# Kernel optimization log

Measured on AMD Instinct MI355X. Metric: run time of the kernel, lower is better.

## Reference

```python
import jax, jax.numpy as jnp
import numpy as np

OUT, IN = 4096, 4096  # W_shape
K, BLOCK = 256, 8     # codebook entries, block dim


def setup_inputs() -> dict:
    key = jax.random.key(0)
    k1, k2, k3, k4, k5 = jax.random.split(key, 5)
    x = jax.random.normal(k1, (4, 2048, IN), dtype=jnp.float32)
    centroids = jax.random.normal(k2, (K, BLOCK), dtype=jnp.float32)
    labels = jax.random.randint(k3, (OUT * IN // BLOCK,), 0, K, dtype=jnp.int64)
    scale = jax.random.uniform(k4, (IN,), dtype=jnp.float32)
    bias = jax.random.normal(k5, (OUT,), dtype=jnp.float32)
    return {"x": x, "centroids": centroids, "labels": labels, "scale": scale, "bias": bias}


def reference(x, centroids, labels, scale, bias):
    # VQ weight decompression: gather codebook vectors, reshape to [OUT, IN]
    W_smooth = centroids[labels].reshape(OUT, IN)
    # F.linear(x * scale, W, bias) == (x*scale) @ W.T + bias
    return jnp.einsum('bsi,oi->bso', x * scale, W_smooth) + bias
```

## Files before the change

### kernel.cpp

```cpp
#include <hip/hip_runtime.h>
#include <stdint.h>

#define M_DIM 8192
#define N_DIM 4096
#define K_DIM 4096
#define NUM_VQ (N_DIM * K_DIM / 8)
#define NUM_X  (M_DIM * K_DIM)

typedef __attribute__((ext_vector_type(4))) float f32x4;
typedef __attribute__((ext_vector_type(8))) short bf16x8;
typedef unsigned short u16;

__device__ inline unsigned short f2bf(float f) {
    union { float f; unsigned int i; } v; v.f = f;
    unsigned int x = v.i;
    return (unsigned short)((x + 0x7FFFu + ((x >> 16) & 1u)) >> 16);
}

__global__ void detect_i64(const int* __restrict__ labels, int* __restrict__ flag) {
    if (threadIdx.x == 0) {
        int is64 = 1;
        for (int i = 1; i < 128; i += 2)
            if (labels[i] != 0) { is64 = 0; break; }
        *flag = is64;
    }
}

__global__ void convert_x(const float* __restrict__ x, u16* __restrict__ xb) {
    int i = blockIdx.x * blockDim.x + threadIdx.x;
    f32x4 a = ((const f32x4*)x)[2 * i];
    f32x4 b = ((const f32x4*)x)[2 * i + 1];
    bf16x8 o;
#pragma unroll
    for (int j = 0; j < 4; ++j) { o[j] = (short)f2bf(a[j]); o[4 + j] = (short)f2bf(b[j]); }
    ((bf16x8*)xb)[i] = o;
}

__global__ void decompress(const int* __restrict__ labels,
                           const float* __restrict__ centroids,
                           const float* __restrict__ scale,
                           u16* __restrict__ Ws,
                           const int* __restrict__ flag) {
    int i = blockIdx.x * blockDim.x + threadIdx.x;
    int lab = (*flag) ? labels[2 * i] : labels[i];
    int kb = i & 511;
    f32x4 c0 = ((const f32x4*)centroids)[2 * lab];
    f32x4 c1 = ((const f32x4*)centroids)[2 * lab + 1];
    f32x4 s0 = ((const f32x4*)scale)[2 * kb];
    f32x4 s1 = ((const f32x4*)scale)[2 * kb + 1];
    bf16x8 o;
#pragma unroll
    for (int j = 0; j < 4; ++j) {
        o[j]     = (short)f2bf(c0[j] * s0[j]);
        o[4 + j] = (short)f2bf(c1[j] * s1[j]);
    }
    ((bf16x8*)Ws)[i] = o;
}

__global__ __launch_bounds__(256)
void gemm_bias(const u16* __restrict__ A, const u16* __restrict__ B,
               const float* __restrict__ bias, float* __restrict__ C) {
    __shared__ u16 ldsA[128 * 32];
    __shared__ u16 ldsB[128 * 32];

    const int tid  = threadIdx.x;
    const int wave = tid >> 6;
    const int lane = tid & 63;
    const int bm = blockIdx.y * 128;
    const int bn = blockIdx.x * 128;

    const int srow = wave * 32 + (lane >> 2);
    const int scol = (lane & 3) * 8;
    const u16* gA = A + (size_t)(bm + srow) * K_DIM + scol;
    const u16* gB = B + (size_t)(bn + srow) * K_DIM + scol;
    u16* lA = ldsA + wave * 1024;
    u16* lB = ldsB + wave * 1024;

    const int wm = (wave >> 1) * 64;
    const int wn = (wave & 1) * 64;
    const int fm = lane & 15;
    const int fk = (lane >> 4) * 8;

    f32x4 acc[4][4];
#pragma unroll
    for (int i = 0; i < 4; ++i)
#pragma unroll
        for (int j = 0; j < 4; ++j)
            acc[i][j] = (f32x4){0.f, 0.f, 0.f, 0.f};

    for (int kt = 0; kt < K_DIM / 32; ++kt) {
        __builtin_amdgcn_global_load_lds(
            (const __attribute__((address_space(1))) void*)gA,
            (__attribute__((address_space(3))) void*)lA, 16, 0, 0);
        __builtin_amdgcn_global_load_lds(
            (const __attribute__((address_space(1))) void*)(gA + 16 * K_DIM),
            (__attribute__((address_space(3))) void*)(lA + 512), 16, 0, 0);
        __builtin_amdgcn_global_load_lds(
            (const __attribute__((address_space(1))) void*)gB,
            (__attribute__((address_space(3))) void*)lB, 16, 0, 0);
        __builtin_amdgcn_global_load_lds(
            (const __attribute__((address_space(1))) void*)(gB + 16 * K_DIM),
            (__attribute__((address_space(3))) void*)(lB + 512), 16, 0, 0);
        gA += 32;
        gB += 32;
        __syncthreads();

        bf16x8 af[4], bfr[4];
#pragma unroll
        for (int i = 0; i < 4; ++i)
            af[i] = *(const bf16x8*)&ldsA[(wm + i * 16 + fm) * 32 + fk];
#pragma unroll
        for (int j = 0; j < 4; ++j)
            bfr[j] = *(const bf16x8*)&ldsB[(wn + j * 16 + fm) * 32 + fk];

#pragma unroll
        for (int i = 0; i < 4; ++i)
#pragma unroll
            for (int j = 0; j < 4; ++j)
                acc[i][j] = __builtin_amdgcn_mfma_f32_16x16x32_bf16(
                    af[i], bfr[j], acc[i][j], 0, 0, 0);
        __syncthreads();
    }

    float biasv[4];
#pragma unroll
    for (int j = 0; j < 4; ++j)
        biasv[j] = bias[bn + wn + j * 16 + (lane & 15)];

    const int crow0 = bm + wm + (lane >> 4) * 4;
    const int ccol0 = bn + wn + (lane & 15);
#pragma unroll
    for (int i = 0; i < 4; ++i)
#pragma unroll
        for (int r = 0; r < 4; ++r) {
            size_t rowoff = (size_t)(crow0 + i * 16 + r) * N_DIM;
#pragma unroll
            for (int j = 0; j < 4; ++j)
                C[rowoff + ccol0 + j * 16] = acc[i][j][r] + biasv[j];
        }
}

__global__ __launch_bounds__(256)
void gemm_bias_cvtA(const float* __restrict__ A32, const u16* __restrict__ B,
                    const float* __restrict__ bias, float* __restrict__ C) {
    __shared__ u16 ldsA[128 * 32];
    __shared__ u16 ldsB[128 * 32];

    const int tid  = threadIdx.x;
    const int wave = tid >> 6;
    const int lane = tid & 63;
    const int bm = blockIdx.y * 128;
    const int bn = blockIdx.x * 128;

    const int srow = wave * 32 + (lane >> 2);
    const int scol = (lane & 3) * 8;
    const float* gA = A32 + (size_t)(bm + srow) * K_DIM + scol;
    const u16*   gB = B   + (size_t)(bn + srow) * K_DIM + scol;
    u16* lA = ldsA + wave * 1024;
    u16* lB = ldsB + wave * 1024;
    const int ldst = lane * 8;

    const int wm = (wave >> 1) * 64;
    const int wn = (wave & 1) * 64;
    const int fm = lane & 15;
    const int fk = (lane >> 4) * 8;

    f32x4 acc[4][4];
#pragma unroll
    for (int i = 0; i < 4; ++i)
#pragma unroll
        for (int j = 0; j < 4; ++j)
            acc[i][j] = (f32x4){0.f, 0.f, 0.f, 0.f};

    for (int kt = 0; kt < K_DIM / 32; ++kt) {
        f32x4 a0 = *(const f32x4*)gA;
        f32x4 a1 = *(const f32x4*)(gA + 4);
        f32x4 a2 = *(const f32x4*)(gA + 16 * K_DIM);
        f32x4 a3 = *(const f32x4*)(gA + 16 * K_DIM + 4);
        __builtin_amdgcn_global_load_lds(
            (const __attribute__((address_space(1))) void*)gB,
            (__attribute__((address_space(3))) void*)lB, 16, 0, 0);
        __builtin_amdgcn_global_load_lds(
            (const __attribute__((address_space(1))) void*)(gB + 16 * K_DIM),
            (__attribute__((address_space(3))) void*)(lB + 512), 16, 0, 0);
        bf16x8 p0, p1;
#pragma unroll
        for (int j = 0; j < 4; ++j) {
            p0[j] = (short)f2bf(a0[j]); p0[4 + j] = (short)f2bf(a1[j]);
            p1[j] = (short)f2bf(a2[j]); p1[4 + j] = (short)f2bf(a3[j]);
        }
        *(bf16x8*)&lA[ldst]       = p0;
        *(bf16x8*)&lA[ldst + 512] = p1;
        gA += 32;
        gB += 32;
        __syncthreads();

        bf16x8 af[4], bfr[4];
#pragma unroll
        for (int i = 0; i < 4; ++i)
            af[i] = *(const bf16x8*)&ldsA[(wm + i * 16 + fm) * 32 + fk];
#pragma unroll
        for (int j = 0; j < 4; ++j)
            bfr[j] = *(const bf16x8*)&ldsB[(wn + j * 16 + fm) * 32 + fk];

#pragma unroll
        for (int i = 0; i < 4; ++i)
#pragma unroll
            for (int j = 0; j < 4; ++j)
                acc[i][j] = __builtin_amdgcn_mfma_f32_16x16x32_bf16(
                    af[i], bfr[j], acc[i][j], 0, 0, 0);
        __syncthreads();
    }

    float biasv[4];
#pragma unroll
    for (int j = 0; j < 4; ++j)
        biasv[j] = bias[bn + wn + j * 16 + (lane & 15)];

    const int crow0 = bm + wm + (lane >> 4) * 4;
    const int ccol0 = bn + wn + (lane & 15);
#pragma unroll
    for (int i = 0; i < 4; ++i)
#pragma unroll
        for (int r = 0; r < 4; ++r) {
            size_t rowoff = (size_t)(crow0 + i * 16 + r) * N_DIM;
#pragma unroll
            for (int j = 0; j < 4; ++j)
                C[rowoff + ccol0 + j * 16] = acc[i][j][r] + biasv[j];
        }
}

extern "C" void kernel_launch(void* const* d_in, const int* in_sizes, int n_in,
                              void* d_out, int out_size, void* d_ws, size_t ws_size,
                              hipStream_t stream) {
    const float* x         = (const float*)d_in[0];
    const float* centroids = (const float*)d_in[1];
    const int*   labels    = (const int*)d_in[2];
    const float* scale     = (const float*)d_in[3];
    const float* bias      = (const float*)d_in[4];
    float* out             = (float*)d_out;

    int* flag = (int*)d_ws;
    u16* Ws   = (u16*)((char*)d_ws + 256);
    u16* Xb   = (u16*)((char*)d_ws + 256 + (size_t)NUM_VQ * 16);

    const size_t need_full = 256 + (size_t)NUM_VQ * 16 + (size_t)NUM_X * 2;
    const size_t need_ws   = 256 + (size_t)NUM_VQ * 16;

    detect_i64<<<1, 64, 0, stream>>>(labels, flag);
    decompress<<<NUM_VQ / 256, 256, 0, stream>>>(labels, centroids, scale, Ws, flag);

    dim3 grid(N_DIM / 128, M_DIM / 128);
    if (ws_size >= need_full) {
        convert_x<<<NUM_X / 8 / 256, 256, 0, stream>>>(x, Xb);
        gemm_bias<<<grid, 256, 0, stream>>>(Xb, Ws, bias, out);
    } else if (ws_size >= need_ws) {
        gemm_bias_cvtA<<<grid, 256, 0, stream>>>(x, Ws, bias, out);
    }
}
```

Before: 536.6 us.

## Swizzle GEMM LDS layout, merge prep kernels, parallelize label-width detect

Applies an XOR swizzle to the column chunk each lane writes into LDS via global_load_lds, and a matching swizzle on the fragment reads, to cut LDS bank conflicts in the MFMA inner loop. It also merges weight decompression and x-to-bf16 conversion into one prep launch, and uses a wave ballot for int64 label detection. The workspace-size fallback path (cvtA GEMM) is removed, so the kernel now assumes a workspace large enough for the bf16 copy of x.

```diff
diff --git a/kernel.cpp b/kernel.cpp
--- a/kernel.cpp
+++ b/kernel.cpp
@@ -6,6 +6,8 @@
 #define K_DIM 4096
 #define NUM_VQ (N_DIM * K_DIM / 8)
 #define NUM_X  (M_DIM * K_DIM)
+#define VQ_BLOCKS (NUM_VQ / 256)
+#define CVT_BLOCKS (NUM_X / 8 / 256)
 
 typedef __attribute__((ext_vector_type(4))) float f32x4;
 typedef __attribute__((ext_vector_type(8))) short bf16x8;
@@ -18,43 +20,42 @@
 }
 
 __global__ void detect_i64(const int* __restrict__ labels, int* __restrict__ flag) {
-    if (threadIdx.x == 0) {
-        int is64 = 1;
-        for (int i = 1; i < 128; i += 2)
-            if (labels[i] != 0) { is64 = 0; break; }
-        *flag = is64;
-    }
+    int v = labels[2 * threadIdx.x + 1];
+    unsigned long long nz = __ballot(v != 0);
+    if (threadIdx.x == 0) *flag = (nz == 0ull) ? 1 : 0;
 }
 
-__global__ void convert_x(const float* __restrict__ x, u16* __restrict__ xb) {
-    int i = blockIdx.x * blockDim.x + threadIdx.x;
-    f32x4 a = ((const f32x4*)x)[2 * i];
-    f32x4 b = ((const f32x4*)x)[2 * i + 1];
-    bf16x8 o;
+__global__ void prep(const int* __restrict__ labels,
+                     const float* __restrict__ centroids,
+                     const float* __restrict__ scale,
+                     const float* __restrict__ x,
+                     u16* __restrict__ Ws, u16* __restrict__ Xb,
+                     const int* __restrict__ flag) {
+    int b = blockIdx.x;
+    if (b < VQ_BLOCKS) {
+        int i = b * 256 + threadIdx.x;
+        int lab = (*flag) ? labels[2 * i] : labels[i];
+        int kb = i & 511;
+        f32x4 c0 = ((const f32x4*)centroids)[2 * lab];
+        f32x4 c1 = ((const f32x4*)centroids)[2 * lab + 1];
+        f32x4 s0 = ((const f32x4*)scale)[2 * kb];
+        f32x4 s1 = ((const f32x4*)scale)[2 * kb + 1];
+        bf16x8 o;
 #pragma unroll
-    for (int j = 0; j < 4; ++j) { o[j] = (short)f2bf(a[j]); o[4 + j] = (short)f2bf(b[j]); }
-    ((bf16x8*)xb)[i] = o;
-}
-
-__global__ void decompress(const int* __restrict__ labels,
-                           const float* __restrict__ centroids,
-                           const float* __restrict__ scale,
-                           u16* __restrict__ Ws,
-                           const int* __restrict__ flag) {
-    int i = blockIdx.x * blockDim.x + threadIdx.x;
-    int lab = (*flag) ? labels[2 * i] : labels[i];
-    int kb = i & 511;
-    f32x4 c0 = ((const f32x4*)centroids)[2 * lab];
-    f32x4 c1 = ((const f32x4*)centroids)[2 * lab + 1];
-    f32x4 s0 = ((const f32x4*)scale)[2 * kb];
-    f32x4 s1 = ((const f32x4*)scale)[2 * kb + 1];
-    bf16x8 o;
+        for (int j = 0; j < 4; ++j) {
+            o[j]     = (short)f2bf(c0[j] * s0[j]);
+            o[4 + j] = (short)f2bf(c1[j] * s1[j]);
+        }
+        ((bf16x8*)Ws)[i] = o;
+    } else {
+        int i = (b - VQ_BLOCKS) * 256 + threadIdx.x;
+        f32x4 a = ((const f32x4*)x)[2 * i];
+        f32x4 c = ((const f32x4*)x)[2 * i + 1];
+        bf16x8 o;
 #pragma unroll
-    for (int j = 0; j < 4; ++j) {
-        o[j]     = (short)f2bf(c0[j] * s0[j]);
-        o[4 + j] = (short)f2bf(c1[j] * s1[j]);
+        for (int j = 0; j < 4; ++j) { o[j] = (short)f2bf(a[j]); o[4 + j] = (short)f2bf(c[j]); }
+        ((bf16x8*)Xb)[i] = o;
     }
-    ((bf16x8*)Ws)[i] = o;
 }
 
 __global__ __launch_bounds__(256)
@@ -70,7 +71,7 @@
     const int bn = blockIdx.x * 128;
 
     const int srow = wave * 32 + (lane >> 2);
-    const int scol = (lane & 3) * 8;
+    const int scol = (((lane & 3) ^ ((lane >> 3) & 3))) * 8;
     const u16* gA = A + (size_t)(bm + srow) * K_DIM + scol;
     const u16* gB = B + (size_t)(bn + srow) * K_DIM + scol;
     u16* lA = ldsA + wave * 1024;
@@ -79,7 +80,7 @@
     const int wm = (wave >> 1) * 64;
     const int wn = (wave & 1) * 64;
     const int fm = lane & 15;
-    const int fk = (lane >> 4) * 8;
+    const int fks = (((lane >> 4) ^ ((lane >> 1) & 3)) & 3) * 8;
 
     f32x4 acc[4][4];
 #pragma unroll
@@ -108,100 +109,10 @@
         bf16x8 af[4], bfr[4];
 #pragma unroll
         for (int i = 0; i < 4; ++i)
-            af[i] = *(const bf16x8*)&ldsA[(wm + i * 16 + fm) * 32 + fk];
+            af[i] = *(const bf16x8*)&ldsA[(wm + i * 16 + fm) * 32 + fks];
 #pragma unroll
         for (int j = 0; j < 4; ++j)
-            bfr[j] = *(const bf16x8*)&ldsB[(wn + j * 16 + fm) * 32 + fk];
-
-#pragma unroll
-        for (int i = 0; i < 4; ++i)
-#pragma unroll
-            for (int j = 0; j < 4; ++j)
-                acc[i][j] = __builtin_amdgcn_mfma_f32_16x16x32_bf16(
-                    af[i], bfr[j], acc[i][j], 0, 0, 0);
-        __syncthreads();
-    }
-
-    float biasv[4];
-#pragma unroll
-    for (int j = 0; j < 4; ++j)
-        biasv[j] = bias[bn + wn + j * 16 + (lane & 15)];
-
-    const int crow0 = bm + wm + (lane >> 4) * 4;
-    const int ccol0 = bn + wn + (lane & 15);
-#pragma unroll
-    for (int i = 0; i < 4; ++i)
-#pragma unroll
-        for (int r = 0; r < 4; ++r) {
-            size_t rowoff = (size_t)(crow0 + i * 16 + r) * N_DIM;
-#pragma unroll
-            for (int j = 0; j < 4; ++j)
-                C[rowoff + ccol0 + j * 16] = acc[i][j][r] + biasv[j];
-        }
-}
-
-__global__ __launch_bounds__(256)
-void gemm_bias_cvtA(const float* __restrict__ A32, const u16* __restrict__ B,
-                    const float* __restrict__ bias, float* __restrict__ C) {
-    __shared__ u16 ldsA[128 * 32];
-    __shared__ u16 ldsB[128 * 32];
-
-    const int tid  = threadIdx.x;
-    const int wave = tid >> 6;
-    const int lane = tid & 63;
-    const int bm = blockIdx.y * 128;
-    const int bn = blockIdx.x * 128;
-
-    const int srow = wave * 32 + (lane >> 2);
-    const int scol = (lane & 3) * 8;
-    const float* gA = A32 + (size_t)(bm + srow) * K_DIM + scol;
-    const u16*   gB = B   + (size_t)(bn + srow) * K_DIM + scol;
-    u16* lA = ldsA + wave * 1024;
-    u16* lB = ldsB + wave * 1024;
-    const int ldst = lane * 8;
-
-    const int wm = (wave >> 1) * 64;
-    const int wn = (wave & 1) * 64;
-    const int fm = lane & 15;
-    const int fk = (lane >> 4) * 8;
-
-    f32x4 acc[4][4];
-#pragma unroll
-    for (int i = 0; i < 4; ++i)
-#pragma unroll
-        for (int j = 0; j < 4; ++j)
-            acc[i][j] = (f32x4){0.f, 0.f, 0.f, 0.f};
-
-    for (int kt = 0; kt < K_DIM / 32; ++kt) {
-        f32x4 a0 = *(const f32x4*)gA;
-        f32x4 a1 = *(const f32x4*)(gA + 4);
-        f32x4 a2 = *(const f32x4*)(gA + 16 * K_DIM);
-        f32x4 a3 = *(const f32x4*)(gA + 16 * K_DIM + 4);
-        __builtin_amdgcn_global_load_lds(
-            (const __attribute__((address_space(1))) void*)gB,
-            (__attribute__((address_space(3))) void*)lB, 16, 0, 0);
-        __builtin_amdgcn_global_load_lds(
-            (const __attribute__((address_space(1))) void*)(gB + 16 * K_DIM),
-            (__attribute__((address_space(3))) void*)(lB + 512), 16, 0, 0);
-        bf16x8 p0, p1;
-#pragma unroll
-        for (int j = 0; j < 4; ++j) {
-            p0[j] = (short)f2bf(a0[j]); p0[4 + j] = (short)f2bf(a1[j]);
-            p1[j] = (short)f2bf(a2[j]); p1[4 + j] = (short)f2bf(a3[j]);
-        }
-        *(bf16x8*)&lA[ldst]       = p0;
-        *(bf16x8*)&lA[ldst + 512] = p1;
-        gA += 32;
-        gB += 32;
-        __syncthreads();
-
-        bf16x8 af[4], bfr[4];
-#pragma unroll
-        for (int i = 0; i < 4; ++i)
-            af[i] = *(const bf16x8*)&ldsA[(wm + i * 16 + fm) * 32 + fk];
-#pragma unroll
-        for (int j = 0; j < 4; ++j)
-            bfr[j] = *(const bf16x8*)&ldsB[(wn + j * 16 + fm) * 32 + fk];
+            bfr[j] = *(const bf16x8*)&ldsB[(wn + j * 16 + fm) * 32 + fks];
 
 #pragma unroll
         for (int i = 0; i < 4; ++i)
@@ -244,17 +155,10 @@
     u16* Ws   = (u16*)((char*)d_ws + 256);
     u16* Xb   = (u16*)((char*)d_ws + 256 + (size_t)NUM_VQ * 16);
 
-    const size_t need_full = 256 + (size_t)NUM_VQ * 16 + (size_t)NUM_X * 2;
-    const size_t need_ws   = 256 + (size_t)NUM_VQ * 16;
-
     detect_i64<<<1, 64, 0, stream>>>(labels, flag);
-    decompress<<<NUM_VQ / 256, 256, 0, stream>>>(labels, centroids, scale, Ws, flag);
+    prep<<<VQ_BLOCKS + CVT_BLOCKS, 256, 0, stream>>>(labels, centroids, scale, x,
+                                                     Ws, Xb, flag);
 
     dim3 grid(N_DIM / 128, M_DIM / 128);
-    if (ws_size >= need_full) {
-        convert_x<<<NUM_X / 8 / 256, 256, 0, stream>>>(x, Xb);
-        gemm_bias<<<grid, 256, 0, stream>>>(Xb, Ws, bias, out);
-    } else if (ws_size >= need_ws) {
-        gemm_bias_cvtA<<<grid, 256, 0, stream>>>(x, Ws, bias, out);
-    }
+    gemm_bias<<<grid, 256, 0, stream>>>(Xb, Ws, bias, out);
 }
```

Result: no change. 538.9 us (+0.4%).
